# Kernel optimization log

Hardware: AMD Instinct MI355X
Metric: run time of the kernel (lower is better)

Reference implementation:

```python
import jax, jax.numpy as jnp
import numpy as np

ATT, WEMB, VIEW, ADIM, EMB = 312, 512, 16, 2048, 2048
B = 2048
IN = ATT + WEMB + VIEW * WEMB  # 9016; output_dim defaults to input_dim
EPS = 1e-8  # torch cosine_similarity eps


def setup_inputs() -> dict:
    key = jax.random.key(0)
    ks = jax.random.split(key, 8)
    s = 0.02
    return {
        "x": jax.random.normal(ks[0], (B, IN), dtype=jnp.float32),
        "Wq": s * jax.random.normal(ks[1], (WEMB, ADIM), dtype=jnp.float32),
        "bq": jnp.zeros((ADIM,), jnp.float32),
        "Wk": s * jax.random.normal(ks[2], (WEMB, ADIM), dtype=jnp.float32),
        "bk": jnp.zeros((ADIM,), jnp.float32),
        "Wv": s * jax.random.normal(ks[3], (WEMB, ADIM), dtype=jnp.float32),
        "bv": jnp.zeros((ADIM,), jnp.float32),
        "Wm": s * jax.random.normal(ks[4], (ATT + ADIM, EMB), dtype=jnp.float32),
        "bm": jnp.zeros((EMB,), jnp.float32),
        "Wd1": s * jax.random.normal(ks[5], (EMB, 4096), dtype=jnp.float32),
        "bd1": jnp.zeros((4096,), jnp.float32),
        "Wd2": s * jax.random.normal(ks[6], (4096, IN), dtype=jnp.float32),
        "bd2": jnp.zeros((IN,), jnp.float32),
    }


def reference(x, Wq, bq, Wk, bk, Wv, bv, Wm, bm, Wd1, bd1, Wd2, bd2):
    att_emb = x[:, :ATT]                                   # [B, 312]
    desc_emb = x[:, ATT:ATT + WEMB]                        # [B, 512]
    gpt_emb = x[:, ATT + WEMB:].reshape(x.shape[0], -1, WEMB)  # [B, V, 512]

    # q is the same projected desc for every view (expand before linear)
    q = desc_emb @ Wq + bq                                 # [B, A]
    k = jnp.einsum("bvw,wa->bva", gpt_emb, Wk) + bk        # [B, V, A]
    v = jnp.einsum("bvw,wa->bva", gpt_emb, Wv) + bv        # [B, V, A]

    # cosed score: cosine similarity * L2 distance
    dot = jnp.einsum("bva,ba->bv", k, q)                   # [B, V]
    qn = jnp.maximum(jnp.linalg.norm(q, axis=-1), EPS)     # [B]
    kn = jnp.maximum(jnp.linalg.norm(k, axis=-1), EPS)     # [B, V]
    cs = dot / (qn[:, None] * kn)
    ed = jnp.linalg.norm(q[:, None, :] - k, axis=-1)       # [B, V]
    attn = jax.nn.softmax(cs * ed, axis=-1)                # [B, V]

    # torch.matmul([B,V], [B,V,A]) -> [B,B,A]; .mean(dim=1) averages over the
    # attn-batch axis, i.e. fused[j] = mean_b(attn[b]) @ v[j]. Compute the
    # mathematically identical form without the BxBxA intermediate.
    attn_mean = attn.mean(axis=0)                          # [V]
    fused = jnp.einsum("v,bva->ba", attn_mean, v)          # [B, A]

    z = jax.nn.relu(jnp.concatenate([att_emb, fused], axis=1) @ Wm + bm)  # [B, EMB]
    h = jax.nn.relu(z @ Wd1 + bd1)                          # [B, 4096]
    return h @ Wd2 + bd2                                    # [B, IN]
```

## Files before the change

### kernel.cpp

```cpp
#include <hip/hip_runtime.h>


typedef __bf16 bf16x8 __attribute__((ext_vector_type(8)));
typedef float  f32x4  __attribute__((ext_vector_type(4)));
typedef unsigned short u16;

#define ATT   312
#define WEMB  512
#define VIEW  16
#define ADIM  2048
#define EMB   2048
#define BATCH 2048
#define INDIM 9016
#define KCAT  2360
#define KCATP 2432
#define NOUT  9016
#define NOUTP 9216

__device__ __forceinline__ u16 f2bf(float f) {
  unsigned u = __builtin_bit_cast(unsigned, f);
  u += 0x7FFFu + ((u >> 16) & 1u);
  return (u16)(u >> 16);
}

__device__ __forceinline__ void gl_lds16(const u16* g, u16* l) {
  __builtin_amdgcn_global_load_lds((const __attribute__((address_space(1))) void*)g,
                                   (__attribute__((address_space(3))) void*)l, 16, 0, 0);
}

__global__ void castx_k(const float* __restrict__ x, u16* __restrict__ cc,
                        u16* __restrict__ desc, u16* __restrict__ gpt) {
  const int b = blockIdx.x, t = threadIdx.x;
  const float4* row = (const float4*)(x + (size_t)b * INDIM);
  for (int c = t; c < INDIM / 4; c += 256) {
    float4 v = row[c];
    ushort4 o = make_ushort4(f2bf(v.x), f2bf(v.y), f2bf(v.z), f2bf(v.w));
    if (c < ATT / 4)                 *(ushort4*)&cc[(size_t)b * KCATP + c * 4] = o;
    else if (c < (ATT + WEMB) / 4)   *(ushort4*)&desc[(size_t)b * WEMB + (c - ATT / 4) * 4] = o;
    else                             *(ushort4*)&gpt[(size_t)b * (VIEW * WEMB) + (c - (ATT + WEMB) / 4) * 4] = o;
  }
}

__global__ void transcast_k(const float* __restrict__ src, u16* __restrict__ dst,
                            int K, int N, int Kp, int Np) {
  __shared__ float tile[64][65];
  const int k0 = blockIdx.y * 64, n0 = blockIdx.x * 64;
  const int t = threadIdx.x;
  const int tr = t >> 4, tc4 = (t & 15) * 4;
#pragma unroll
  for (int i = 0; i < 4; ++i) {
    const int k = k0 + tr + i * 16;
    float v0 = 0.f, v1 = 0.f, v2 = 0.f, v3 = 0.f;
    if (k < K) {
      const int n = n0 + tc4;
      const float* p = src + (size_t)k * N + n;
      if (n + 3 < N) { float4 v = *(const float4*)p; v0 = v.x; v1 = v.y; v2 = v.z; v3 = v.w; }
      else {
        if (n + 0 < N) v0 = p[0];
        if (n + 1 < N) v1 = p[1];
        if (n + 2 < N) v2 = p[2];
        if (n + 3 < N) v3 = p[3];
      }
    }
    tile[tr + i * 16][tc4 + 0] = v0;
    tile[tr + i * 16][tc4 + 1] = v1;
    tile[tr + i * 16][tc4 + 2] = v2;
    tile[tr + i * 16][tc4 + 3] = v3;
  }
  __syncthreads();
#pragma unroll
  for (int i = 0; i < 4; ++i) {
    const int rn = tr + i * 16;
    const int n = n0 + rn;
    const int kk = k0 + tc4;
    if (n < Np) {
      const bool nv = (n < N);
      ushort4 o = make_ushort4(f2bf(nv ? tile[tc4 + 0][rn] : 0.f),
                               f2bf(nv ? tile[tc4 + 1][rn] : 0.f),
                               f2bf(nv ? tile[tc4 + 2][rn] : 0.f),
                               f2bf(nv ? tile[tc4 + 3][rn] : 0.f));
      *(ushort4*)&dst[(size_t)n * Kp + kk] = o;
    }
  }
}

__device__ __forceinline__ void stage_half(const u16* __restrict__ src, int ld,
                                           u16* dst, int wave, int lane) {
#pragma unroll
  for (int j = 0; j < 2; ++j) {
    const int s = wave * 2 + j;
    const int r = ((s >> 1) << 4) + (lane >> 2);
    const int c = ((s & 1) << 5) +
                  (((lane & 3) << 3) ^ (((lane >> 5) & 1) << 4));
    gl_lds16(src + (long)r * ld + c, dst + s * 512 + (lane << 3));
  }
}

#define BAR   __builtin_amdgcn_s_barrier()
#define LGKM0 asm volatile("s_waitcnt lgkmcnt(0)" ::: "memory")
#define VM6   asm volatile("s_waitcnt vmcnt(6)" ::: "memory")
#define VM4   asm volatile("s_waitcnt vmcnt(4)" ::: "memory")
#define VM0   asm volatile("s_waitcnt vmcnt(0)" ::: "memory")

#define RDA(bufo, lo, hi) do { _Pragma("unroll") for (int mf = (lo); mf <= (hi); ++mf) \
  _Pragma("unroll") for (int kk = 0; kk < 2; ++kk) \
    a[mf][kk] = *(const bf16x8*)&lds[(bufo) + aoff0 + (mf * 2 + kk) * 512]; } while (0)
#define RDB(bufo, lo, hi) do { _Pragma("unroll") for (int nf = (lo); nf <= (hi); ++nf) \
  _Pragma("unroll") for (int kk = 0; kk < 2; ++kk) \
    b[nf][kk] = *(const bf16x8*)&lds[(bufo) + boff0 + nf * 1024 + kk * 512]; } while (0)
#define QUAD(qm, qn) do { __builtin_amdgcn_s_setprio(1); \
  _Pragma("unroll") for (int m4 = 0; m4 < 4; ++m4) \
  _Pragma("unroll") for (int n2 = 0; n2 < 2; ++n2) \
  _Pragma("unroll") for (int kk = 0; kk < 2; ++kk) \
    acc[(qm) * 4 + m4][(qn) * 2 + n2] = __builtin_amdgcn_mfma_f32_16x16x32_bf16( \
        a[(qm) * 4 + m4][kk], b[(qn) * 2 + n2][kk], acc[(qm) * 4 + m4][(qn) * 2 + n2], 0, 0, 0); \
  __builtin_amdgcn_s_setprio(0); } while (0)

template <int MODE, bool RELU>
__global__ __launch_bounds__(512, 2)
void gemm256(const u16* __restrict__ A, const u16* __restrict__ BT,
             const float* __restrict__ bias, int K, int Nreal,
             float* __restrict__ dstF, u16* __restrict__ dstH, int ldc,
             const float* __restrict__ qbuf, float* __restrict__ dotb,
             float* __restrict__ kn2b, int mt, int nt, int fastm) {
  __shared__ alignas(16) u16 lds[65536];
  const int nwg = mt * nt;
  const int xcd = blockIdx.x & 7, idx = blockIdx.x >> 3;
  const int qq = nwg >> 3, rr = nwg & 7;
  const int wg = (xcd < rr ? xcd * (qq + 1) : rr * (qq + 1) + (xcd - rr) * qq) + idx;
  int tm, tn;
  if (fastm) { tm = wg % mt; tn = wg / mt; } else { tn = wg % nt; tm = wg / nt; }

  const int tid = threadIdx.x;
  const int wave = tid >> 6, lane = tid & 63;
  const long m0 = (long)tm * 256, n0 = (long)tn * 256;
  const int wm = wave >> 2, wn = wave & 3;
  const u16* Ab = A + m0 * K;
  const u16* Bb = BT + n0 * K;

  f32x4 acc[8][4] = {};
  bf16x8 a[8][2], b[4][2];
  const int LP = (lane & 15) * 32 + ((((lane >> 4) << 3)) ^ (((lane >> 3) & 1) << 4));
  const int aoff0 = wm * 8192 + LP;
  const int boff0 = 16384 + (wn >> 1) * 8192 + (wn & 1) * 4096 + LP;
  const int NT = K >> 6;

  stage_half(Ab,                K, &lds[0],     wave, lane);
  stage_half(Ab + 128 * K,      K, &lds[8192],  wave, lane);
  stage_half(Bb,                K, &lds[16384], wave, lane);
  stage_half(Bb + 128 * K,      K, &lds[24576], wave, lane);
  stage_half(Ab + 64,           K, &lds[32768], wave, lane);
  stage_half(Ab + 128 * K + 64, K, &lds[40960], wave, lane);
  stage_half(Bb + 64,           K, &lds[49152], wave, lane);
  VM6; BAR;

  const int iters = NT >> 1;
  for (int i = 0; i < iters; ++i) {
    const int t0 = 2 * i;
    const bool nl = (i < iters - 1);
    RDA(0, 0, 3); RDB(0, 0, 1);
    stage_half(Bb + 128 * K + (t0 + 1) * 64, K, &lds[57344], wave, lane);
    BAR; LGKM0; QUAD(0, 0); BAR;
    RDA(0, 4, 7);
    BAR; LGKM0; QUAD(1, 0); BAR;
    RDB(0, 2, 3);
    if (nl) stage_half(Ab + (t0 + 2) * 64, K, &lds[0], wave, lane);
    BAR; LGKM0; QUAD(0, 1); BAR;
    if (nl) stage_half(Ab + 128 * K + (t0 + 2) * 64, K, &lds[8192], wave, lane);
    BAR; QUAD(1, 1);
    if (nl) { VM4; } else { VM0; }
    BAR;
    RDA(32768, 0, 3); RDB(32768, 0, 1);
    if (nl) stage_half(Bb + (t0 + 2) * 64, K, &lds[16384], wave, lane);
    BAR; LGKM0; QUAD(0, 0); BAR;
    RDA(32768, 4, 7);
    if (nl) stage_half(Bb + 128 * K + (t0 + 2) * 64, K, &lds[24576], wave, lane);
    BAR; LGKM0; QUAD(1, 0); BAR;
    RDB(32768, 2, 3);
    if (nl) stage_half(Ab + (t0 + 3) * 64, K, &lds[32768], wave, lane);
    BAR; LGKM0; QUAD(0, 1); BAR;
    if (nl) {
      stage_half(Ab + 128 * K + (t0 + 3) * 64, K, &lds[40960], wave, lane);
      stage_half(Bb + (t0 + 3) * 64, K, &lds[49152], wave, lane);
    }
    BAR; QUAD(1, 1);
    if (nl) VM6;
    BAR;
  }

  const int lr = lane >> 4, lc = lane & 15;
  if (MODE == 2) {
#pragma unroll
    for (int mf = 0; mf < 8; ++mf) {
#pragma unroll
      for (int r = 0; r < 4; ++r) {
        const long grow = m0 + wm * 128 + mf * 16 + lr * 4 + r;
        const long bb = grow >> 4;
        float ds = 0.f, ks2 = 0.f;
#pragma unroll
        for (int nf = 0; nf < 4; ++nf) {
          const long col = n0 + wn * 64 + nf * 16 + lc;
          float kv = acc[mf][nf][r] + bias[col];
          ds += kv * qbuf[bb * ADIM + col];
          ks2 += kv * kv;
        }
#pragma unroll
        for (int m = 1; m < 16; m <<= 1) {
          ds += __shfl_xor(ds, m, 64);
          ks2 += __shfl_xor(ks2, m, 64);
        }
        if (lc == 0) {
          atomicAdd(&dotb[grow], ds);
          atomicAdd(&kn2b[grow], ks2);
        }
      }
    }
  } else {
#pragma unroll
    for (int mf = 0; mf < 8; ++mf) {
#pragma unroll
      for (int nf = 0; nf < 4; ++nf) {
        const long col = n0 + wn * 64 + nf * 16 + lc;
        if (col < Nreal) {
          const float bv_ = bias[col];
#pragma unroll
          for (int r = 0; r < 4; ++r) {
            const long row = m0 + wm * 128 + mf * 16 + lr * 4 + r;
            float v = acc[mf][nf][r] + bv_;
            if (RELU) v = fmaxf(v, 0.f);
            if (MODE == 0) dstF[row * (long)ldc + col] = v;
            else           dstH[row * (long)ldc + col] = f2bf(v);
          }
        }
      }
    }
  }
}

template <int MODE, bool RELU>
__global__ __launch_bounds__(256, 2)
void gemm_bt(const u16* __restrict__ A, const u16* __restrict__ BT,
             const float* __restrict__ bias, int K, int Nreal,
             float* __restrict__ dstF, u16* __restrict__ dstH, int ldc,
             int mt, int nt, int fastm) {
  __shared__ alignas(16) u16 Ash[128 * 64];
  __shared__ alignas(16) u16 Bsh[128 * 64];
  const int nwg = mt * nt;
  const int xcd = blockIdx.x & 7, idx = blockIdx.x >> 3;
  const int qq = nwg >> 3, rr = nwg & 7;
  const int wg = (xcd < rr ? xcd * (qq + 1) : rr * (qq + 1) + (xcd - rr) * qq) + idx;
  int tm, tn;
  if (fastm) { tm = wg % mt; tn = wg / mt; } else { tn = wg % nt; tm = wg / nt; }

  const int tid = threadIdx.x;
  const int wave = tid >> 6, lane = tid & 63;
  const long m0 = (long)tm * 128;
  const long n0 = (long)tn * 128;
  const int wm = wave >> 1, wnn = wave & 1;
  f32x4 acc[4][4] = {};

  const int srow = (wave << 5) + (lane >> 3);
  const int scol = (lane & 7) << 3;

  for (int k0 = 0; k0 < K; k0 += 64) {
    __syncthreads();
#pragma unroll
    for (int i = 0; i < 4; ++i) {
      const int r = srow + i * 8;
      gl_lds16(A + (m0 + r) * (long)K + k0 + scol, &Ash[r * 64 + scol]);
      gl_lds16(BT + (n0 + r) * (long)K + k0 + scol, &Bsh[r * 64 + scol]);
    }
    __syncthreads();
#pragma unroll
    for (int kb = 0; kb < 2; ++kb) {
      bf16x8 af[4], bfv[4];
#pragma unroll
      for (int f = 0; f < 4; ++f) {
        af[f]  = *(const bf16x8*)&Ash[(wm * 64 + f * 16 + (lane & 15)) * 64 + kb * 32 + (lane >> 4) * 8];
        bfv[f] = *(const bf16x8*)&Bsh[(wnn * 64 + f * 16 + (lane & 15)) * 64 + kb * 32 + (lane >> 4) * 8];
      }
#pragma unroll
      for (int mf = 0; mf < 4; ++mf)
#pragma unroll
        for (int nf = 0; nf < 4; ++nf)
          acc[mf][nf] = __builtin_amdgcn_mfma_f32_16x16x32_bf16(af[mf], bfv[nf], acc[mf][nf], 0, 0, 0);
    }
  }

  const int lr = lane >> 4, lc = lane & 15;
#pragma unroll
  for (int mf = 0; mf < 4; ++mf) {
#pragma unroll
    for (int nf = 0; nf < 4; ++nf) {
      const long col = n0 + wnn * 64 + nf * 16 + lc;
      if (col < Nreal) {
        const float bv_ = bias[col];
#pragma unroll
        for (int r = 0; r < 4; ++r) {
          const long row = m0 + wm * 64 + mf * 16 + lr * 4 + r;
          float v = acc[mf][nf][r] + bv_;
          if (RELU) v = fmaxf(v, 0.f);
          if (MODE == 0) dstF[row * (long)ldc + col] = v;
          else           dstH[row * (long)ldc + col] = f2bf(v);
        }
      }
    }
  }
}

__global__ void qnorm_k(const float* __restrict__ q, float* __restrict__ qn2) {
  const int b = blockIdx.x, t = threadIdx.x;
  const float4* row = (const float4*)(q + (size_t)b * ADIM);
  float s = 0.f;
#pragma unroll
  for (int i = 0; i < 2; ++i) {
    float4 v = row[t + i * 256];
    s += v.x * v.x + v.y * v.y + v.z * v.z + v.w * v.w;
  }
#pragma unroll
  for (int m = 1; m < 64; m <<= 1) s += __shfl_xor(s, m, 64);
  __shared__ float wsum[4];
  if ((t & 63) == 0) wsum[t >> 6] = s;
  __syncthreads();
  if (t == 0) qn2[b] = wsum[0] + wsum[1] + wsum[2] + wsum[3];
}

__global__ void attn_k(const float* __restrict__ dotb, const float* __restrict__ kn2b,
                       const float* __restrict__ qn2, float* __restrict__ asum) {
  const int b = blockIdx.x * 256 + threadIdx.x;
  const int lane = threadIdx.x & 63;
  const float q2 = qn2[b];
  const float qn = fmaxf(sqrtf(q2), 1e-8f);
  float lg[VIEW];
  float mx = -1e30f;
#pragma unroll
  for (int v = 0; v < VIEW; ++v) {
    const float d = dotb[b * VIEW + v], k2 = kn2b[b * VIEW + v];
    const float kn = fmaxf(sqrtf(k2), 1e-8f);
    const float cs = d / (qn * kn);
    const float ed = sqrtf(fmaxf(q2 - 2.f * d + k2, 0.f));
    lg[v] = cs * ed;
    mx = fmaxf(mx, lg[v]);
  }
  float s = 0.f;
#pragma unroll
  for (int v = 0; v < VIEW; ++v) { lg[v] = expf(lg[v] - mx); s += lg[v]; }
  const float inv = 1.f / s;
#pragma unroll
  for (int v = 0; v < VIEW; ++v) {
    float aa = lg[v] * inv;
#pragma unroll
    for (int m = 1; m < 64; m <<= 1) aa += __shfl_xor(aa, m, 64);
    if (lane == 0) atomicAdd(&asum[v], aa);
  }
}

__global__ void gtilde_k(const u16* __restrict__ gpt, const float* __restrict__ asum,
                         u16* __restrict__ g) {
  const int b = blockIdx.x, t = threadIdx.x;
  float am[VIEW];
#pragma unroll
  for (int v = 0; v < VIEW; ++v) am[v] = asum[v] * (1.f / (float)BATCH);
  float s[8] = {};
  const u16* gx = gpt + (size_t)b * (VIEW * WEMB) + t * 8;
#pragma unroll
  for (int v = 0; v < VIEW; ++v) {
    bf16x8 gv = *(const bf16x8*)&gx[v * WEMB];
#pragma unroll
    for (int j = 0; j < 8; ++j) s[j] += am[v] * (float)gv[j];
  }
  ushort4 o0, o1;
  o0 = make_ushort4(f2bf(s[0]), f2bf(s[1]), f2bf(s[2]), f2bf(s[3]));
  o1 = make_ushort4(f2bf(s[4]), f2bf(s[5]), f2bf(s[6]), f2bf(s[7]));
  *(ushort4*)&g[(size_t)b * WEMB + t * 8] = o0;
  *(ushort4*)&g[(size_t)b * WEMB + t * 8 + 4] = o1;
}

extern "C" void kernel_launch(void* const* d_in, const int* in_sizes, int n_in,
                              void* d_out, int out_size, void* d_ws, size_t ws_size,
                              hipStream_t stream) {
  const float* x   = (const float*)d_in[0];
  const float* Wq  = (const float*)d_in[1];
  const float* bq  = (const float*)d_in[2];
  const float* Wk  = (const float*)d_in[3];
  const float* bk  = (const float*)d_in[4];
  const float* Wv  = (const float*)d_in[5];
  const float* bv  = (const float*)d_in[6];
  const float* Wm  = (const float*)d_in[7];
  const float* bm  = (const float*)d_in[8];
  const float* Wd1 = (const float*)d_in[9];
  const float* bd1 = (const float*)d_in[10];
  const float* Wd2 = (const float*)d_in[11];
  const float* bd2 = (const float*)d_in[12];
  float* out = (float*)d_out;

  char* ws = (char*)d_ws;
  size_t off = 0;
  auto alloc = [&](size_t bytes) -> void* {
    void* p = ws + off;
    off = (off + bytes + 255) & ~(size_t)255;
    return p;
  };
  u16* WqT  = (u16*)alloc((size_t)ADIM * WEMB * 2);
  u16* WkT  = (u16*)alloc((size_t)ADIM * WEMB * 2);
  u16* WvT  = (u16*)alloc((size_t)ADIM * WEMB * 2);
  u16* WmT  = (u16*)alloc((size_t)EMB * KCATP * 2);
  u16* Wd1T = (u16*)alloc((size_t)4096 * EMB * 2);
  u16* Wd2T = (u16*)alloc((size_t)NOUTP * 4096 * 2);
  u16* desc = (u16*)alloc((size_t)BATCH * WEMB * 2);
  u16* gpt  = (u16*)alloc((size_t)BATCH * VIEW * WEMB * 2);
  u16* cc   = (u16*)alloc((size_t)BATCH * KCATP * 2);
  float* q    = (float*)alloc((size_t)BATCH * ADIM * 4);
  float* qn2  = (float*)alloc((size_t)BATCH * 4);
  float* stats = (float*)alloc((size_t)(BATCH * VIEW * 2 + 64) * 4);
  float* dotb = stats;
  float* kn2b = stats + BATCH * VIEW;
  float* asum = stats + BATCH * VIEW * 2;
  u16* gt = (u16*)alloc((size_t)BATCH * WEMB * 2);
  u16* z  = (u16*)alloc((size_t)BATCH * EMB * 2);
  u16* h  = (u16*)alloc((size_t)BATCH * 4096 * 2);
  if (off > ws_size) return;

  hipMemsetAsync(stats, 0, (size_t)(BATCH * VIEW * 2 + 64) * 4, stream);
  hipMemsetAsync(cc, 0, (size_t)BATCH * KCATP * 2, stream);

  castx_k<<<BATCH, 256, 0, stream>>>(x, cc, desc, gpt);

  transcast_k<<<dim3(ADIM / 64, WEMB / 64), 256, 0, stream>>>(Wq, WqT, WEMB, ADIM, WEMB, ADIM);
  transcast_k<<<dim3(ADIM / 64, WEMB / 64), 256, 0, stream>>>(Wk, WkT, WEMB, ADIM, WEMB, ADIM);
  transcast_k<<<dim3(ADIM / 64, WEMB / 64), 256, 0, stream>>>(Wv, WvT, WEMB, ADIM, WEMB, ADIM);
  transcast_k<<<dim3(EMB / 64, KCATP / 64), 256, 0, stream>>>(Wm, WmT, KCAT, EMB, KCATP, EMB);
  transcast_k<<<dim3(4096 / 64, EMB / 64), 256, 0, stream>>>(Wd1, Wd1T, EMB, 4096, EMB, 4096);
  transcast_k<<<dim3(NOUTP / 64, 4096 / 64), 256, 0, stream>>>(Wd2, Wd2T, 4096, NOUT, 4096, NOUTP);

  gemm_bt<0, false><<<16 * 16, 256, 0, stream>>>(
      desc, WqT, bq, WEMB, ADIM, q, nullptr, ADIM, BATCH / 128, ADIM / 128, 0);
  qnorm_k<<<BATCH, 256, 0, stream>>>(q, qn2);
  gemm256<2, false><<<128 * 8, 512, 0, stream>>>(
      gpt, WkT, bk, WEMB, ADIM, nullptr, nullptr, 0, q, dotb, kn2b,
      BATCH * VIEW / 256, ADIM / 256, 0);
  attn_k<<<BATCH / 256, 256, 0, stream>>>(dotb, kn2b, qn2, asum);
  gtilde_k<<<BATCH, 64, 0, stream>>>(gpt, asum, gt);
  gemm_bt<1, false><<<16 * 16, 256, 0, stream>>>(
      gt, WvT, bv, WEMB, ADIM, nullptr, cc + ATT, KCATP, BATCH / 128, ADIM / 128, 0);
  gemm_bt<1, true><<<16 * 16, 256, 0, stream>>>(
      cc, WmT, bm, KCATP, EMB, nullptr, z, EMB, BATCH / 128, EMB / 128, 0);
  gemm256<1, true><<<8 * 16, 512, 0, stream>>>(
      z, Wd1T, bd1, EMB, 4096, nullptr, h, 4096, nullptr, nullptr, nullptr,
      BATCH / 256, 4096 / 256, 1);
  gemm256<0, false><<<8 * 36, 512, 0, stream>>>(
      h, Wd2T, bd2, 4096, NOUT, out, nullptr, NOUT, nullptr, nullptr, nullptr,
      BATCH / 256, NOUTP / 256, 1);
}
```

Baseline: 708.1 us.

## Split-K the final decoder GEMM, merge weight transposes, drop cc memset

The final h@Wd2 GEMM is split along K into two halves, so twice as many workgroups run, which fills more CUs than the previous 288 tiles. The first half writes into out with bias and the second into a scratch fp32 buffer aliased onto earlier workspace, and a separate add kernel sums them. The six weight transpose/cast launches are merged into one kernel driven by a descriptor table. The full memset of cc is replaced by zeroing only its pad columns inside castx. The cost is an extra fp32 partial write plus a read-modify-write pass over the output.

```diff
diff --git a/kernel.cpp b/kernel.cpp
--- a/kernel.cpp
+++ b/kernel.cpp
@@ -39,27 +39,38 @@
     else if (c < (ATT + WEMB) / 4)   *(ushort4*)&desc[(size_t)b * WEMB + (c - ATT / 4) * 4] = o;
     else                             *(ushort4*)&gpt[(size_t)b * (VIEW * WEMB) + (c - (ATT + WEMB) / 4) * 4] = o;
   }
-}
-
-__global__ void transcast_k(const float* __restrict__ src, u16* __restrict__ dst,
-                            int K, int N, int Kp, int Np) {
+  if (t < (KCATP - KCAT) / 4) {
+    *(ushort4*)&cc[(size_t)b * KCATP + KCAT + t * 4] = make_ushort4(0, 0, 0, 0);
+  }
+}
+
+struct TcDesc { const float* src; u16* dst; int K, N, Kp, Np, ntx, base; };
+struct TcArgs { TcDesc d[6]; };
+
+__global__ void transcast6_k(TcArgs A) {
   __shared__ float tile[64][65];
-  const int k0 = blockIdx.y * 64, n0 = blockIdx.x * 64;
+  int mi = 0;
+  const int bid = blockIdx.x;
+#pragma unroll
+  for (int i = 1; i < 6; ++i) if (bid >= A.d[i].base) mi = i;
+  const TcDesc& D = A.d[mi];
+  const int local = bid - D.base;
+  const int n0 = (local % D.ntx) * 64, k0 = (local / D.ntx) * 64;
   const int t = threadIdx.x;
   const int tr = t >> 4, tc4 = (t & 15) * 4;
 #pragma unroll
   for (int i = 0; i < 4; ++i) {
     const int k = k0 + tr + i * 16;
     float v0 = 0.f, v1 = 0.f, v2 = 0.f, v3 = 0.f;
-    if (k < K) {
+    if (k < D.K) {
       const int n = n0 + tc4;
-      const float* p = src + (size_t)k * N + n;
-      if (n + 3 < N) { float4 v = *(const float4*)p; v0 = v.x; v1 = v.y; v2 = v.z; v3 = v.w; }
+      const float* p = D.src + (size_t)k * D.N + n;
+      if (n + 3 < D.N) { float4 v = *(const float4*)p; v0 = v.x; v1 = v.y; v2 = v.z; v3 = v.w; }
       else {
-        if (n + 0 < N) v0 = p[0];
-        if (n + 1 < N) v1 = p[1];
-        if (n + 2 < N) v2 = p[2];
-        if (n + 3 < N) v3 = p[3];
+        if (n + 0 < D.N) v0 = p[0];
+        if (n + 1 < D.N) v1 = p[1];
+        if (n + 2 < D.N) v2 = p[2];
+        if (n + 3 < D.N) v3 = p[3];
       }
     }
     tile[tr + i * 16][tc4 + 0] = v0;
@@ -73,13 +84,13 @@
     const int rn = tr + i * 16;
     const int n = n0 + rn;
     const int kk = k0 + tc4;
-    if (n < Np) {
-      const bool nv = (n < N);
+    if (n < D.Np && kk < D.Kp) {
+      const bool nv = (n < D.N);
       ushort4 o = make_ushort4(f2bf(nv ? tile[tc4 + 0][rn] : 0.f),
                                f2bf(nv ? tile[tc4 + 1][rn] : 0.f),
                                f2bf(nv ? tile[tc4 + 2][rn] : 0.f),
                                f2bf(nv ? tile[tc4 + 3][rn] : 0.f));
-      *(ushort4*)&dst[(size_t)n * Kp + kk] = o;
+      *(ushort4*)&D.dst[(size_t)n * D.Kp + kk] = o;
     }
   }
 }
@@ -120,30 +131,34 @@
 __global__ __launch_bounds__(512, 2)
 void gemm256(const u16* __restrict__ A, const u16* __restrict__ BT,
              const float* __restrict__ bias, int K, int Nreal,
-             float* __restrict__ dstF, u16* __restrict__ dstH, int ldc,
+             float* __restrict__ dstF, u16* __restrict__ dstH,
+             float* __restrict__ PF, int ldc,
              const float* __restrict__ qbuf, float* __restrict__ dotb,
-             float* __restrict__ kn2b, int mt, int nt, int fastm) {
+             float* __restrict__ kn2b, int mt, int nt, int fastm,
+             int ks, int kl) {
   __shared__ alignas(16) u16 lds[65536];
-  const int nwg = mt * nt;
+  const int nwg = mt * nt * ks;
   const int xcd = blockIdx.x & 7, idx = blockIdx.x >> 3;
   const int qq = nwg >> 3, rr = nwg & 7;
   const int wg = (xcd < rr ? xcd * (qq + 1) : rr * (qq + 1) + (xcd - rr) * qq) + idx;
+  const int ksl = wg % ks;
+  const int rem = wg / ks;
   int tm, tn;
-  if (fastm) { tm = wg % mt; tn = wg / mt; } else { tn = wg % nt; tm = wg / nt; }
+  if (fastm) { tm = rem % mt; tn = rem / mt; } else { tn = rem % nt; tm = rem / nt; }
 
   const int tid = threadIdx.x;
   const int wave = tid >> 6, lane = tid & 63;
   const long m0 = (long)tm * 256, n0 = (long)tn * 256;
   const int wm = wave >> 2, wn = wave & 3;
-  const u16* Ab = A + m0 * K;
-  const u16* Bb = BT + n0 * K;
+  const u16* Ab = A + m0 * K + (long)ksl * kl;
+  const u16* Bb = BT + n0 * K + (long)ksl * kl;
 
   f32x4 acc[8][4] = {};
   bf16x8 a[8][2], b[4][2];
   const int LP = (lane & 15) * 32 + ((((lane >> 4) << 3)) ^ (((lane >> 3) & 1) << 4));
   const int aoff0 = wm * 8192 + LP;
   const int boff0 = 16384 + (wn >> 1) * 8192 + (wn & 1) * 4096 + LP;
-  const int NT = K >> 6;
+  const int NT = kl >> 6;
 
   stage_half(Ab,                K, &lds[0],     wave, lane);
   stage_half(Ab + 128 * K,      K, &lds[8192],  wave, lane);
@@ -215,6 +230,23 @@
         }
       }
     }
+  } else if (MODE == 4) {
+    float* base = (ksl == 0) ? dstF : PF;
+#pragma unroll
+    for (int mf = 0; mf < 8; ++mf) {
+#pragma unroll
+      for (int nf = 0; nf < 4; ++nf) {
+        const long col = n0 + wn * 64 + nf * 16 + lc;
+        if (col < Nreal) {
+          const float bv_ = (ksl == 0) ? bias[col] : 0.f;
+#pragma unroll
+          for (int r = 0; r < 4; ++r) {
+            const long row = m0 + wm * 128 + mf * 16 + lr * 4 + r;
+            base[row * (long)ldc + col] = acc[mf][nf][r] + bv_;
+          }
+        }
+      }
+    }
   } else {
 #pragma unroll
     for (int mf = 0; mf < 8; ++mf) {
@@ -235,6 +267,14 @@
       }
     }
   }
+}
+
+__global__ void addf_k(float* __restrict__ out, const float* __restrict__ p) {
+  const size_t i = ((size_t)blockIdx.x * 256 + threadIdx.x) * 4;
+  float4 a = *(float4*)&out[i];
+  float4 b = *(const float4*)&p[i];
+  a.x += b.x; a.y += b.y; a.z += b.z; a.w += b.w;
+  *(float4*)&out[i] = a;
 }
 
 template <int MODE, bool RELU>
@@ -418,27 +458,35 @@
   float* asum = stats + BATCH * VIEW * 2;
   u16* gt = (u16*)alloc((size_t)BATCH * WEMB * 2);
   u16* z  = (u16*)alloc((size_t)BATCH * EMB * 2);
+  (void)alloc((size_t)1 << 20);
   u16* h  = (u16*)alloc((size_t)BATCH * 4096 * 2);
   if (off > ws_size) return;
+  float* Pout = (float*)desc;
 
   hipMemsetAsync(stats, 0, (size_t)(BATCH * VIEW * 2 + 64) * 4, stream);
-  hipMemsetAsync(cc, 0, (size_t)BATCH * KCATP * 2, stream);
 
   castx_k<<<BATCH, 256, 0, stream>>>(x, cc, desc, gpt);
 
-  transcast_k<<<dim3(ADIM / 64, WEMB / 64), 256, 0, stream>>>(Wq, WqT, WEMB, ADIM, WEMB, ADIM);
-  transcast_k<<<dim3(ADIM / 64, WEMB / 64), 256, 0, stream>>>(Wk, WkT, WEMB, ADIM, WEMB, ADIM);
-  transcast_k<<<dim3(ADIM / 64, WEMB / 64), 256, 0, stream>>>(Wv, WvT, WEMB, ADIM, WEMB, ADIM);
-  transcast_k<<<dim3(EMB / 64, KCATP / 64), 256, 0, stream>>>(Wm, WmT, KCAT, EMB, KCATP, EMB);
-  transcast_k<<<dim3(4096 / 64, EMB / 64), 256, 0, stream>>>(Wd1, Wd1T, EMB, 4096, EMB, 4096);
-  transcast_k<<<dim3(NOUTP / 64, 4096 / 64), 256, 0, stream>>>(Wd2, Wd2T, 4096, NOUT, 4096, NOUTP);
+  TcArgs ta;
+  int base = 0;
+  auto setd = [&](int i, const float* s, u16* d, int K, int N, int Kp, int Np) {
+    ta.d[i] = TcDesc{s, d, K, N, Kp, Np, (Np + 63) / 64, base};
+    base += ((Np + 63) / 64) * ((Kp + 63) / 64);
+  };
+  setd(0, Wq, WqT, WEMB, ADIM, WEMB, ADIM);
+  setd(1, Wk, WkT, WEMB, ADIM, WEMB, ADIM);
+  setd(2, Wv, WvT, WEMB, ADIM, WEMB, ADIM);
+  setd(3, Wm, WmT, KCAT, EMB, KCATP, EMB);
+  setd(4, Wd1, Wd1T, EMB, 4096, EMB, 4096);
+  setd(5, Wd2, Wd2T, 4096, NOUT, 4096, NOUTP);
+  transcast6_k<<<base, 256, 0, stream>>>(ta);
 
   gemm_bt<0, false><<<16 * 16, 256, 0, stream>>>(
       desc, WqT, bq, WEMB, ADIM, q, nullptr, ADIM, BATCH / 128, ADIM / 128, 0);
   qnorm_k<<<BATCH, 256, 0, stream>>>(q, qn2);
   gemm256<2, false><<<128 * 8, 512, 0, stream>>>(
-      gpt, WkT, bk, WEMB, ADIM, nullptr, nullptr, 0, q, dotb, kn2b,
-      BATCH * VIEW / 256, ADIM / 256, 0);
+      gpt, WkT, bk, WEMB, ADIM, nullptr, nullptr, nullptr, 0, q, dotb, kn2b,
+      BATCH * VIEW / 256, ADIM / 256, 0, 1, WEMB);
   attn_k<<<BATCH / 256, 256, 0, stream>>>(dotb, kn2b, qn2, asum);
   gtilde_k<<<BATCH, 64, 0, stream>>>(gpt, asum, gt);
   gemm_bt<1, false><<<16 * 16, 256, 0, stream>>>(
@@ -446,9 +494,10 @@
   gemm_bt<1, true><<<16 * 16, 256, 0, stream>>>(
       cc, WmT, bm, KCATP, EMB, nullptr, z, EMB, BATCH / 128, EMB / 128, 0);
   gemm256<1, true><<<8 * 16, 512, 0, stream>>>(
-      z, Wd1T, bd1, EMB, 4096, nullptr, h, 4096, nullptr, nullptr, nullptr,
-      BATCH / 256, 4096 / 256, 1);
-  gemm256<0, false><<<8 * 36, 512, 0, stream>>>(
-      h, Wd2T, bd2, 4096, NOUT, out, nullptr, NOUT, nullptr, nullptr, nullptr,
-      BATCH / 256, NOUTP / 256, 1);
-}
+      z, Wd1T, bd1, EMB, 4096, nullptr, h, nullptr, 4096, nullptr, nullptr, nullptr,
+      BATCH / 256, 4096 / 256, 1, 1, EMB);
+  gemm256<4, false><<<8 * 36 * 2, 512, 0, stream>>>(
+      h, Wd2T, bd2, 4096, NOUT, out, nullptr, Pout, NOUT, nullptr, nullptr, nullptr,
+      BATCH / 256, NOUTP / 256, 1, 2, 2048);
+  addf_k<<<(BATCH * NOUT) / 1024, 256, 0, stream>>>(out, Pout);
+}
```

Result: faster. 690.4 us (-2.5%).
